# Performance work log

Hardware: AMD Instinct MI355X
Metric: run time of the kernel (lower is better)

The kernel has to match this reference:

```python
import jax, jax.numpy as jnp
import numpy as np

N_NODES = 50000
N_EDGES = 800000
IN_CH, HID_CH, OUT_CH, HEADS = 64, 32, 64, 8
NEG_SLOPE = 0.2


def setup_inputs() -> dict:
    key = jax.random.key(0)
    ks = jax.random.split(key, 12)
    x = jax.random.normal(ks[0], (N_NODES, IN_CH), dtype=jnp.float32)
    src = jax.random.randint(ks[1], (N_EDGES,), 0, N_NODES)
    dst = jax.random.randint(ks[2], (N_EDGES,), 0, N_NODES)
    edge_index = jnp.stack([src, dst]).astype(jnp.int64)
    g1 = 1.0 / np.sqrt(IN_CH)
    g2 = 1.0 / np.sqrt(HID_CH * HEADS)
    W1 = jax.random.normal(ks[3], (IN_CH, HEADS * HID_CH), dtype=jnp.float32) * g1
    a1_src = jax.random.normal(ks[4], (HEADS, HID_CH), dtype=jnp.float32) * g1
    a1_dst = jax.random.normal(ks[5], (HEADS, HID_CH), dtype=jnp.float32) * g1
    b1 = jnp.zeros((HEADS * HID_CH,), dtype=jnp.float32)
    W2 = jax.random.normal(ks[6], (HEADS * HID_CH, OUT_CH), dtype=jnp.float32) * g2
    a2_src = jax.random.normal(ks[7], (1, OUT_CH), dtype=jnp.float32) * g2
    a2_dst = jax.random.normal(ks[8], (1, OUT_CH), dtype=jnp.float32) * g2
    b2 = jnp.zeros((OUT_CH,), dtype=jnp.float32)
    return {"x": x, "edge_index": edge_index, "W1": W1, "a1_src": a1_src,
            "a1_dst": a1_dst, "b1": b1, "W2": W2, "a2_src": a2_src,
            "a2_dst": a2_dst, "b2": b2}


def _gat_conv(x, src, dst, W, a_s, a_d, b, heads, out_ch, concat):
    """PyG GATConv: per-head linear, edge attention, segment softmax, scatter-add."""
    n = x.shape[0]
    h = (x @ W).reshape(n, heads, out_ch)                    # [N,H,C]
    al_s = jnp.einsum('nhc,hc->nh', h, a_s)                  # [N,H]
    al_d = jnp.einsum('nhc,hc->nh', h, a_d)
    e = jax.nn.leaky_relu(al_s[src] + al_d[dst], NEG_SLOPE)  # [E,H]
    m = jax.ops.segment_max(e, dst, num_segments=n)          # [N,H]
    m = jnp.where(jnp.isfinite(m), m, 0.0)
    ex = jnp.exp(e - m[dst])
    denom = jax.ops.segment_sum(ex, dst, num_segments=n)
    alpha = ex / (denom[dst] + 1e-16)                        # [E,H]
    msg = h[src] * alpha[:, :, None]                         # [E,H,C]
    out = jax.ops.segment_sum(msg, dst, num_segments=n)      # [N,H,C]
    out = out.reshape(n, heads * out_ch) if concat else out.mean(axis=1)
    return out + b


def reference(x, edge_index, W1, a1_src, a1_dst, b1, W2, a2_src, a2_dst, b2):
    n = x.shape[0]
    loops = jnp.arange(n, dtype=edge_index.dtype)
    src = jnp.concatenate([edge_index[0], loops])  # self-loops (PyG default)
    dst = jnp.concatenate([edge_index[1], loops])
    h = _gat_conv(x, src, dst, W1, a1_src, a1_dst, b1, HEADS, HID_CH, True)
    h = jax.nn.elu(h)
    return _gat_conv(h, src, dst, W2, a2_src, a2_dst, b2, 1, OUT_CH, False)
```

## Files before the change

kernel.cpp:

```cpp
#include <hip/hip_runtime.h>
#include <hip/hip_fp16.h>

#define NEG_SLOPE 0.2f
#define EPB 4096
#define CAP_B 2560

__global__ __launch_bounds__(256, 4) void k_phase1(
    const int* __restrict__ ei, int E,
    const float* __restrict__ x, const float* __restrict__ W1,
    const float* __restrict__ a1s, const float* __restrict__ a1d,
    __half* __restrict__ h1h, float* __restrict__ al1s, float* __restrict__ al1d,
    int* __restrict__ cursor, unsigned* __restrict__ pairs,
    int n, int nbuck, int nP1B)
{
  __shared__ int sh[2048];
  int t = threadIdx.x;
  if (blockIdx.x < nP1B) {
    int* hist = sh;
    int* hbase = sh + 512;
    for (int i = t; i < nbuck; i += 256) hist[i] = 0;
    __syncthreads();
    int ebase = blockIdx.x * EPB;
    int pk[16], bk[16], rk[16];
#pragma unroll
    for (int k = 0; k < 16; k++) {
      int eid = ebase + k * 256 + t;
      bk[k] = -1; pk[k] = 0; rk[k] = 0;
      if (eid < E) {
        int s = ei[eid], d = ei[E + eid];
        s = (s < 0) ? 0 : (s >= n ? n - 1 : s);
        d = (d < 0) ? 0 : (d >= n ? n - 1 : d);
        bk[k] = d >> 7;
        pk[k] = ((d & 127) << 17) | s;
        rk[k] = atomicAdd(&hist[d >> 7], 1);
      }
    }
    __syncthreads();
    for (int b = t; b < nbuck; b += 256) {
      int c = hist[b];
      hbase[b] = c ? atomicAdd(&cursor[b], c) : 0;
    }
    __syncthreads();
#pragma unroll
    for (int k = 0; k < 16; k++) {
      if (bk[k] >= 0) {
        int idx = hbase[bk[k]] + rk[k];
        if (idx < CAP_B)
          pairs[(size_t)bk[k] * CAP_B + idx] = (unsigned)pk[k];
      }
    }
    return;
  }
  float (*xs)[64] = reinterpret_cast<float(*)[64]>(sh);
  int cg = t & 63;
  int mg = t >> 6;
  int base = (blockIdx.x - nP1B) * 32;
  for (int i = t; i < 32 * 16; i += 256) {
    int m = i >> 4, k4 = i & 15;
    int node = base + m;
    float4 v = make_float4(0.f, 0.f, 0.f, 0.f);
    if (node < n) v = reinterpret_cast<const float4*>(x + (size_t)node * 64)[k4];
    reinterpret_cast<float4*>(&xs[m][0])[k4] = v;
  }
  float4 as4 = reinterpret_cast<const float4*>(a1s)[cg];
  float4 ad4 = reinterpret_cast<const float4*>(a1d)[cg];
  __syncthreads();
  float4 acc[8];
#pragma unroll
  for (int m = 0; m < 8; m++) acc[m] = make_float4(0.f, 0.f, 0.f, 0.f);
#pragma unroll 1
  for (int k4 = 0; k4 < 16; k4++) {
    float4 w0 = reinterpret_cast<const float4*>(W1 + (size_t)(4 * k4 + 0) * 256)[cg];
    float4 w1 = reinterpret_cast<const float4*>(W1 + (size_t)(4 * k4 + 1) * 256)[cg];
    float4 w2 = reinterpret_cast<const float4*>(W1 + (size_t)(4 * k4 + 2) * 256)[cg];
    float4 w3 = reinterpret_cast<const float4*>(W1 + (size_t)(4 * k4 + 3) * 256)[cg];
#pragma unroll
    for (int m = 0; m < 8; m++) {
      float4 xv = reinterpret_cast<float4*>(&xs[mg * 8 + m][0])[k4];
      acc[m].x = fmaf(xv.x, w0.x, acc[m].x); acc[m].y = fmaf(xv.x, w0.y, acc[m].y);
      acc[m].z = fmaf(xv.x, w0.z, acc[m].z); acc[m].w = fmaf(xv.x, w0.w, acc[m].w);
      acc[m].x = fmaf(xv.y, w1.x, acc[m].x); acc[m].y = fmaf(xv.y, w1.y, acc[m].y);
      acc[m].z = fmaf(xv.y, w1.z, acc[m].z); acc[m].w = fmaf(xv.y, w1.w, acc[m].w);
      acc[m].x = fmaf(xv.z, w2.x, acc[m].x); acc[m].y = fmaf(xv.z, w2.y, acc[m].y);
      acc[m].z = fmaf(xv.z, w2.z, acc[m].z); acc[m].w = fmaf(xv.z, w2.w, acc[m].w);
      acc[m].x = fmaf(xv.w, w3.x, acc[m].x); acc[m].y = fmaf(xv.w, w3.y, acc[m].y);
      acc[m].z = fmaf(xv.w, w3.z, acc[m].z); acc[m].w = fmaf(xv.w, w3.w, acc[m].w);
    }
  }
#pragma unroll
  for (int m = 0; m < 8; m++) {
    int node = base + mg * 8 + m;
    if (node < n) {
      int head = cg >> 3;
      __half2 p01 = __floats2half2_rn(acc[m].x, acc[m].y);
      __half2 p23 = __floats2half2_rn(acc[m].z, acc[m].w);
      uint2 pko;
      pko.x = *reinterpret_cast<unsigned int*>(&p01);
      pko.y = *reinterpret_cast<unsigned int*>(&p23);
      reinterpret_cast<uint2*>(h1h + (size_t)head * n * 32 + (size_t)node * 32)[cg & 7] = pko;
      float s_ = acc[m].x * as4.x + acc[m].y * as4.y + acc[m].z * as4.z + acc[m].w * as4.w;
      float d_ = acc[m].x * ad4.x + acc[m].y * ad4.y + acc[m].z * ad4.z + acc[m].w * ad4.w;
      s_ += __shfl_xor(s_, 1); d_ += __shfl_xor(d_, 1);
      s_ += __shfl_xor(s_, 2); d_ += __shfl_xor(d_, 2);
      s_ += __shfl_xor(s_, 4); d_ += __shfl_xor(d_, 4);
      if ((cg & 7) == 0) {
        al1s[(size_t)head * n + node] = s_;
        al1d[(size_t)head * n + node] = d_;
      }
    }
  }
}

__global__ __launch_bounds__(256) void k_pass2(
    const unsigned* __restrict__ pairs, const int* __restrict__ cursor,
    int* __restrict__ gcur, int* __restrict__ deg, int* __restrict__ rowoff,
    int* __restrict__ csr, int n)
{
  __shared__ int cnt[128], off[128], rk[128];
  __shared__ int bbase;
  int b = blockIdx.x, t = threadIdx.x;
  if (t < 128) { cnt[t] = 0; rk[t] = 0; }
  __syncthreads();
  int total = min(cursor[b], CAP_B);
  size_t base = (size_t)b * CAP_B;
  for (int i = t; i < total; i += 256)
    atomicAdd(&cnt[pairs[base + i] >> 17], 1);
  __syncthreads();
  if (t == 0) {
    int run = 0;
    for (int i = 0; i < 128; i++) { off[i] = run; run += cnt[i]; }
    bbase = atomicAdd(gcur, run);
  }
  __syncthreads();
  int bb = bbase;
  if (t < 128) {
    int node = (b << 7) + t;
    if (node < n) { deg[node] = cnt[t]; rowoff[node] = bb + off[t]; }
  }
  for (int i = t; i < total; i += 256) {
    unsigned p = pairs[base + i];
    int local = p >> 17;
    int slot = atomicAdd(&rk[local], 1);
    csr[bb + off[local] + slot] = (int)(p & 0x1FFFF);
  }
}

__global__ __launch_bounds__(256, 4) void k_linear2(
    const __half* __restrict__ hacth, const float* __restrict__ W2,
    const float* __restrict__ a2s, const float* __restrict__ a2d,
    __half* __restrict__ h2h, float* __restrict__ al2s, float* __restrict__ al2d,
    int n)
{
  __shared__ float xs[32][260];
  int t = threadIdx.x;
  int cg = t & 15;
  int mg = t >> 4;
  int base = blockIdx.x * 32;
  for (int i = t; i < 32 * 32; i += 256) {
    int m = i >> 5, c8 = i & 31;
    int node = base + m;
    uint4 pk = make_uint4(0, 0, 0, 0);
    if (node < n) pk = reinterpret_cast<const uint4*>(hacth + (size_t)node * 256)[c8];
    __half2* hp = reinterpret_cast<__half2*>(&pk);
    float2 f0 = __half22float2(hp[0]);
    float2 f1 = __half22float2(hp[1]);
    float2 f2 = __half22float2(hp[2]);
    float2 f3 = __half22float2(hp[3]);
    float4* dst = reinterpret_cast<float4*>(&xs[m][c8 * 8]);
    dst[0] = make_float4(f0.x, f0.y, f1.x, f1.y);
    dst[1] = make_float4(f2.x, f2.y, f3.x, f3.y);
  }
  float4 as4 = reinterpret_cast<const float4*>(a2s)[cg];
  float4 ad4 = reinterpret_cast<const float4*>(a2d)[cg];
  __syncthreads();
  float4 a0 = make_float4(0.f, 0.f, 0.f, 0.f);
  float4 a1 = make_float4(0.f, 0.f, 0.f, 0.f);
#pragma unroll 2
  for (int k4 = 0; k4 < 64; k4++) {
    float4 w0 = reinterpret_cast<const float4*>(W2 + (size_t)(4 * k4 + 0) * 64)[cg];
    float4 w1 = reinterpret_cast<const float4*>(W2 + (size_t)(4 * k4 + 1) * 64)[cg];
    float4 w2 = reinterpret_cast<const float4*>(W2 + (size_t)(4 * k4 + 2) * 64)[cg];
    float4 w3 = reinterpret_cast<const float4*>(W2 + (size_t)(4 * k4 + 3) * 64)[cg];
    float4 x0 = *reinterpret_cast<float4*>(&xs[2 * mg + 0][k4 * 4]);
    float4 x1 = *reinterpret_cast<float4*>(&xs[2 * mg + 1][k4 * 4]);
    a0.x = fmaf(x0.x, w0.x, a0.x); a0.y = fmaf(x0.x, w0.y, a0.y);
    a0.z = fmaf(x0.x, w0.z, a0.z); a0.w = fmaf(x0.x, w0.w, a0.w);
    a0.x = fmaf(x0.y, w1.x, a0.x); a0.y = fmaf(x0.y, w1.y, a0.y);
    a0.z = fmaf(x0.y, w1.z, a0.z); a0.w = fmaf(x0.y, w1.w, a0.w);
    a0.x = fmaf(x0.z, w2.x, a0.x); a0.y = fmaf(x0.z, w2.y, a0.y);
    a0.z = fmaf(x0.z, w2.z, a0.z); a0.w = fmaf(x0.z, w2.w, a0.w);
    a0.x = fmaf(x0.w, w3.x, a0.x); a0.y = fmaf(x0.w, w3.y, a0.y);
    a0.z = fmaf(x0.w, w3.z, a0.z); a0.w = fmaf(x0.w, w3.w, a0.w);
    a1.x = fmaf(x1.x, w0.x, a1.x); a1.y = fmaf(x1.x, w0.y, a1.y);
    a1.z = fmaf(x1.x, w0.z, a1.z); a1.w = fmaf(x1.x, w0.w, a1.w);
    a1.x = fmaf(x1.y, w1.x, a1.x); a1.y = fmaf(x1.y, w1.y, a1.y);
    a1.z = fmaf(x1.y, w1.z, a1.z); a1.w = fmaf(x1.y, w1.w, a1.w);
    a1.x = fmaf(x1.z, w2.x, a1.x); a1.y = fmaf(x1.z, w2.y, a1.y);
    a1.z = fmaf(x1.z, w2.z, a1.z); a1.w = fmaf(x1.z, w2.w, a1.w);
    a1.x = fmaf(x1.w, w3.x, a1.x); a1.y = fmaf(x1.w, w3.y, a1.y);
    a1.z = fmaf(x1.w, w3.z, a1.z); a1.w = fmaf(x1.w, w3.w, a1.w);
  }
#pragma unroll
  for (int nd = 0; nd < 2; nd++) {
    float4 a = nd ? a1 : a0;
    int node = base + 2 * mg + nd;
    if (node < n) {
      __half2 q0 = __floats2half2_rn(a.x, a.y);
      __half2 q1 = __floats2half2_rn(a.z, a.w);
      uint2 pk;
      pk.x = *reinterpret_cast<unsigned int*>(&q0);
      pk.y = *reinterpret_cast<unsigned int*>(&q1);
      reinterpret_cast<uint2*>(h2h + (size_t)node * 64)[cg] = pk;
      float s_ = a.x * as4.x + a.y * as4.y + a.z * as4.z + a.w * as4.w;
      float d_ = a.x * ad4.x + a.y * ad4.y + a.z * ad4.z + a.w * ad4.w;
      s_ += __shfl_xor(s_, 1); d_ += __shfl_xor(d_, 1);
      s_ += __shfl_xor(s_, 2); d_ += __shfl_xor(d_, 2);
      s_ += __shfl_xor(s_, 4); d_ += __shfl_xor(d_, 4);
      s_ += __shfl_xor(s_, 8); d_ += __shfl_xor(d_, 8);
      if (cg == 0) { al2s[node] = s_; al2d[node] = d_; }
    }
  }
}

__global__ __launch_bounds__(256) void k_gather1(
    const __half* __restrict__ h1h, const float* __restrict__ al1s, const float* __restrict__ al1d,
    const int* __restrict__ degv, const int* __restrict__ rowoff, const int* __restrict__ csr,
    const float* __restrict__ b1, __half* __restrict__ hacth, int n)
{
  int head = blockIdx.x & 7;
  int node = ((blockIdx.x >> 3) << 6) + (threadIdx.x >> 2);
  if (node >= n) return;
  int q = threadIdx.x & 2 ? (threadIdx.x & 3) : (threadIdx.x & 3);
  q = threadIdx.x & 3;
  const __half* slab = h1h + (size_t)head * n * 32;
  const float* als = al1s + (size_t)head * n;
  float ald = al1d[(size_t)head * n + node];
  int beg = rowoff[node];
  int deg = degv[node];
  uint4 nr = reinterpret_cast<const uint4*>(slab + (size_t)node * 32)[q];
  float eS = als[node] + ald;
  eS = eS > 0.f ? eS : NEG_SLOPE * eS;
  float exS = __expf(eS);
  float acc[8];
#pragma unroll
  for (int k = 0; k < 8; k++) acc[k] = 0.f;
  float den = 0.f;
  if (deg > 0) {
    int sA = csr[beg];
    float alA = als[sA];
    uint4 pa = reinterpret_cast<const uint4*>(slab + (size_t)sA * 32)[q];
    for (int i = 0; i < deg; i++) {
      float alB = 0.f;
      uint4 pb = make_uint4(0, 0, 0, 0);
      if (i + 1 < deg) {
        int sB = csr[beg + i + 1];
        alB = als[sB];
        pb = reinterpret_cast<const uint4*>(slab + (size_t)sB * 32)[q];
      }
      float e = alA + ald;
      e = e > 0.f ? e : NEG_SLOPE * e;
      float ex = __expf(e);
      den += ex;
      __half2* hp = reinterpret_cast<__half2*>(&pa);
#pragma unroll
      for (int j = 0; j < 4; j++) {
        float2 f = __half22float2(hp[j]);
        acc[2 * j + 0] = fmaf(ex, f.x, acc[2 * j + 0]);
        acc[2 * j + 1] = fmaf(ex, f.y, acc[2 * j + 1]);
      }
      alA = alB; pa = pb;
    }
  }
  den += exS;
  {
    __half2* hp = reinterpret_cast<__half2*>(&nr);
#pragma unroll
    for (int j = 0; j < 4; j++) {
      float2 f = __half22float2(hp[j]);
      acc[2 * j + 0] = fmaf(exS, f.x, acc[2 * j + 0]);
      acc[2 * j + 1] = fmaf(exS, f.y, acc[2 * j + 1]);
    }
  }
  float inv = 1.f / (den + 1e-16f);
  float4 b40 = reinterpret_cast<const float4*>(b1 + head * 32)[2 * q];
  float4 b41 = reinterpret_cast<const float4*>(b1 + head * 32)[2 * q + 1];
  float o[8];
  o[0] = acc[0] * inv + b40.x; o[1] = acc[1] * inv + b40.y;
  o[2] = acc[2] * inv + b40.z; o[3] = acc[3] * inv + b40.w;
  o[4] = acc[4] * inv + b41.x; o[5] = acc[5] * inv + b41.y;
  o[6] = acc[6] * inv + b41.z; o[7] = acc[7] * inv + b41.w;
#pragma unroll
  for (int k = 0; k < 8; k++) o[k] = o[k] > 0.f ? o[k] : (__expf(o[k]) - 1.f);
  uint4 w0;
  __half2 t0, t1;
  t0 = __floats2half2_rn(o[0], o[1]);  w0.x = *reinterpret_cast<unsigned int*>(&t0);
  t1 = __floats2half2_rn(o[2], o[3]);  w0.y = *reinterpret_cast<unsigned int*>(&t1);
  t0 = __floats2half2_rn(o[4], o[5]);  w0.z = *reinterpret_cast<unsigned int*>(&t0);
  t1 = __floats2half2_rn(o[6], o[7]);  w0.w = *reinterpret_cast<unsigned int*>(&t1);
  *reinterpret_cast<uint4*>(hacth + (size_t)node * 256 + head * 32 + q * 8) = w0;
}

__global__ __launch_bounds__(256) void k_gather2(
    const __half* __restrict__ h2h, const float* __restrict__ al2s, const float* __restrict__ al2d,
    const int* __restrict__ degv, const int* __restrict__ rowoff, const int* __restrict__ csr,
    const float* __restrict__ b2, float* __restrict__ out, int n)
{
  int node = blockIdx.x * 32 + (threadIdx.x >> 3);
  if (node >= n) return;
  int q = threadIdx.x & 7;
  int beg = rowoff[node];
  int deg = degv[node];
  float ald = al2d[node];
  uint4 pN = reinterpret_cast<const uint4*>(h2h + (size_t)node * 64)[q];
  float eS = al2s[node] + ald;
  eS = eS > 0.f ? eS : NEG_SLOPE * eS;
  float exS = __expf(eS);
  float acc[8];
#pragma unroll
  for (int k = 0; k < 8; k++) acc[k] = 0.f;
  float den = 0.f;
  if (deg > 0) {
    int sA = csr[beg];
    float alA = al2s[sA];
    uint4 pA = reinterpret_cast<const uint4*>(h2h + (size_t)sA * 64)[q];
    for (int i = 0; i < deg; i++) {
      float alB = 0.f;
      uint4 pB = make_uint4(0, 0, 0, 0);
      if (i + 1 < deg) {
        int sB = csr[beg + i + 1];
        alB = al2s[sB];
        pB = reinterpret_cast<const uint4*>(h2h + (size_t)sB * 64)[q];
      }
      float e = alA + ald;
      e = e > 0.f ? e : NEG_SLOPE * e;
      float ex = __expf(e);
      den += ex;
      __half2* hp = reinterpret_cast<__half2*>(&pA);
#pragma unroll
      for (int j = 0; j < 4; j++) {
        float2 f = __half22float2(hp[j]);
        acc[2 * j + 0] = fmaf(ex, f.x, acc[2 * j + 0]);
        acc[2 * j + 1] = fmaf(ex, f.y, acc[2 * j + 1]);
      }
      alA = alB; pA = pB;
    }
  }
  den += exS;
  {
    __half2* hp = reinterpret_cast<__half2*>(&pN);
#pragma unroll
    for (int j = 0; j < 4; j++) {
      float2 f = __half22float2(hp[j]);
      acc[2 * j + 0] = fmaf(exS, f.x, acc[2 * j + 0]);
      acc[2 * j + 1] = fmaf(exS, f.y, acc[2 * j + 1]);
    }
  }
  float inv = 1.f / (den + 1e-16f);
  float4 b40 = reinterpret_cast<const float4*>(b2)[2 * q];
  float4 b41 = reinterpret_cast<const float4*>(b2)[2 * q + 1];
  float4 o0, o1;
  o0.x = acc[0] * inv + b40.x; o0.y = acc[1] * inv + b40.y;
  o0.z = acc[2] * inv + b40.z; o0.w = acc[3] * inv + b40.w;
  o1.x = acc[4] * inv + b41.x; o1.y = acc[5] * inv + b41.y;
  o1.z = acc[6] * inv + b41.z; o1.w = acc[7] * inv + b41.w;
  float4* orow = reinterpret_cast<float4*>(out + (size_t)node * 64);
  orow[2 * q] = o0; orow[2 * q + 1] = o1;
}

extern "C" void kernel_launch(void* const* d_in, const int* in_sizes, int n_in,
                              void* d_out, int out_size, void* d_ws, size_t ws_size,
                              hipStream_t stream)
{
  const float* x        = (const float*)d_in[0];
  const int*   ei       = (const int*)d_in[1];
  const float* W1       = (const float*)d_in[2];
  const float* a1s      = (const float*)d_in[3];
  const float* a1d      = (const float*)d_in[4];
  const float* b1       = (const float*)d_in[5];
  const float* W2       = (const float*)d_in[6];
  const float* a2s      = (const float*)d_in[7];
  const float* a2d      = (const float*)d_in[8];
  const float* b2       = (const float*)d_in[9];
  float* out            = (float*)d_out;

  int N  = in_sizes[0] / 64;
  int E  = in_sizes[1] / 2;
  int NBUCK = (N + 127) >> 7;

  char* p = (char*)d_ws;
  auto alloc = [&](size_t bytes) -> char* {
    char* r = p;
    p += (bytes + 255) & ~(size_t)255;
    return r;
  };
  __half* h1h    = (__half*)alloc((size_t)N * 256 * 2);
  __half* hacth  = (__half*)alloc((size_t)N * 256 * 2);
  float* al1s    = (float*)alloc((size_t)N * 8 * 4);
  float* al1d    = (float*)alloc((size_t)N * 8 * 4);
  float* al2s    = (float*)alloc((size_t)N * 4);
  float* al2d    = (float*)alloc((size_t)N * 4);
  int*   deg     = (int*)alloc((size_t)N * 4);
  int*   rowoff  = (int*)alloc((size_t)N * 4);
  int*   csr     = (int*)alloc((size_t)NBUCK * CAP_B * 4);
  unsigned* pairs = (unsigned*)alloc((size_t)NBUCK * CAP_B * 4);
  int*   cursor  = (int*)alloc((size_t)(NBUCK + 1) * 4);
  int*   gcur    = cursor + NBUCK;
  __half* h2h    = h1h;

  hipMemsetAsync(cursor, 0, (size_t)(NBUCK + 1) * 4, stream);

  int nP1B = (E + EPB - 1) / EPB;
  int nLB = (N + 31) / 32;
  k_phase1<<<nP1B + nLB, 256, 0, stream>>>(ei, E, x, W1, a1s, a1d,
                                           h1h, al1s, al1d, cursor, pairs, N, NBUCK, nP1B);
  k_pass2<<<NBUCK, 256, 0, stream>>>(pairs, cursor, gcur, deg, rowoff, csr, N);
  int nG1 = 8 * ((N + 63) / 64);
  k_gather1<<<nG1, 256, 0, stream>>>(h1h, al1s, al1d, deg, rowoff, csr, b1, hacth, N);
  k_linear2<<<(N + 31) / 32, 256, 0, stream>>>(hacth, W2, a2s, a2d, h2h, al2s, al2d, N);
  k_gather2<<<(N + 31) / 32, 256, 0, stream>>>(h2h, al2s, al2d, deg, rowoff, csr, b2, out, N);
}
```

Measured before the change: 232.7 us.

## Split layer-2 features into channel slabs and widen per-thread gather work

Layer-2 linear output is now stored as two 32-channel half-precision slabs, so gather2 splits channels across blocks the way gather1 splits heads, giving a smaller per-slab working set for the random row reads. Both gather kernels now use 2 threads per node with 16 channels each instead of 4 or 8 threads, and prefetch the next CSR index one step further ahead. The CSR index loads and the output stores become nontemporal. This cuts redundant index and attention-logit loads per lane, at the cost of more registers per thread and fewer threads per node.

After: 323.8 us. +39.2%, slower.

```diff
diff --git a/kernel.cpp b/kernel.cpp
--- a/kernel.cpp
+++ b/kernel.cpp
@@ -4,6 +4,9 @@
 #define NEG_SLOPE 0.2f
 #define EPB 4096
 #define CAP_B 2560
+
+typedef unsigned int uint4v __attribute__((ext_vector_type(4)));
+typedef float float4v __attribute__((ext_vector_type(4)));
 
 __global__ __launch_bounds__(256, 4) void k_phase1(
     const int* __restrict__ ei, int E,
@@ -210,7 +213,7 @@
       uint2 pk;
       pk.x = *reinterpret_cast<unsigned int*>(&q0);
       pk.y = *reinterpret_cast<unsigned int*>(&q1);
-      reinterpret_cast<uint2*>(h2h + (size_t)node * 64)[cg] = pk;
+      reinterpret_cast<uint2*>(h2h + (size_t)(cg >> 3) * n * 32 + (size_t)node * 32)[cg & 7] = pk;
       float s_ = a.x * as4.x + a.y * as4.y + a.z * as4.z + a.w * as4.w;
       float d_ = a.x * ad4.x + a.y * ad4.y + a.z * ad4.z + a.w * ad4.w;
       s_ += __shfl_xor(s_, 1); d_ += __shfl_xor(d_, 1);
@@ -228,76 +231,97 @@
     const float* __restrict__ b1, __half* __restrict__ hacth, int n)
 {
   int head = blockIdx.x & 7;
-  int node = ((blockIdx.x >> 3) << 6) + (threadIdx.x >> 2);
+  int node = ((blockIdx.x >> 3) << 7) + (threadIdx.x >> 1);
   if (node >= n) return;
-  int q = threadIdx.x & 2 ? (threadIdx.x & 3) : (threadIdx.x & 3);
-  q = threadIdx.x & 3;
+  int q = threadIdx.x & 1;
   const __half* slab = h1h + (size_t)head * n * 32;
   const float* als = al1s + (size_t)head * n;
   float ald = al1d[(size_t)head * n + node];
   int beg = rowoff[node];
   int deg = degv[node];
-  uint4 nr = reinterpret_cast<const uint4*>(slab + (size_t)node * 32)[q];
+  const uint4* rowN = reinterpret_cast<const uint4*>(slab + (size_t)node * 32);
+  uint4 n0 = rowN[2 * q], n1 = rowN[2 * q + 1];
   float eS = als[node] + ald;
   eS = eS > 0.f ? eS : NEG_SLOPE * eS;
   float exS = __expf(eS);
-  float acc[8];
-#pragma unroll
-  for (int k = 0; k < 8; k++) acc[k] = 0.f;
+  float acc[16];
+#pragma unroll
+  for (int k = 0; k < 16; k++) acc[k] = 0.f;
   float den = 0.f;
   if (deg > 0) {
-    int sA = csr[beg];
-    float alA = als[sA];
-    uint4 pa = reinterpret_cast<const uint4*>(slab + (size_t)sA * 32)[q];
+    int s1 = (deg > 1) ? __builtin_nontemporal_load(csr + beg + 1) : 0;
+    int s0 = __builtin_nontemporal_load(csr + beg);
+    float alA = als[s0];
+    const uint4* rA = reinterpret_cast<const uint4*>(slab + (size_t)s0 * 32);
+    uint4 pa0 = rA[2 * q], pa1 = rA[2 * q + 1];
     for (int i = 0; i < deg; i++) {
+      int sN = 0;
+      if (i + 2 < deg) sN = __builtin_nontemporal_load(csr + beg + i + 2);
       float alB = 0.f;
-      uint4 pb = make_uint4(0, 0, 0, 0);
+      uint4 pb0 = make_uint4(0, 0, 0, 0), pb1 = make_uint4(0, 0, 0, 0);
       if (i + 1 < deg) {
-        int sB = csr[beg + i + 1];
-        alB = als[sB];
-        pb = reinterpret_cast<const uint4*>(slab + (size_t)sB * 32)[q];
+        alB = als[s1];
+        const uint4* rB = reinterpret_cast<const uint4*>(slab + (size_t)s1 * 32);
+        pb0 = rB[2 * q]; pb1 = rB[2 * q + 1];
       }
       float e = alA + ald;
       e = e > 0.f ? e : NEG_SLOPE * e;
       float ex = __expf(e);
       den += ex;
-      __half2* hp = reinterpret_cast<__half2*>(&pa);
+      __half2* hp0 = reinterpret_cast<__half2*>(&pa0);
+      __half2* hp1 = reinterpret_cast<__half2*>(&pa1);
 #pragma unroll
       for (int j = 0; j < 4; j++) {
-        float2 f = __half22float2(hp[j]);
-        acc[2 * j + 0] = fmaf(ex, f.x, acc[2 * j + 0]);
-        acc[2 * j + 1] = fmaf(ex, f.y, acc[2 * j + 1]);
-      }
-      alA = alB; pa = pb;
+        float2 f0 = __half22float2(hp0[j]);
+        float2 f1 = __half22float2(hp1[j]);
+        acc[2 * j + 0] = fmaf(ex, f0.x, acc[2 * j + 0]);
+        acc[2 * j + 1] = fmaf(ex, f0.y, acc[2 * j + 1]);
+        acc[8 + 2 * j + 0] = fmaf(ex, f1.x, acc[8 + 2 * j + 0]);
+        acc[8 + 2 * j + 1] = fmaf(ex, f1.y, acc[8 + 2 * j + 1]);
+      }
+      alA = alB; pa0 = pb0; pa1 = pb1; s1 = sN;
     }
   }
   den += exS;
   {
-    __half2* hp = reinterpret_cast<__half2*>(&nr);
+    __half2* hp0 = reinterpret_cast<__half2*>(&n0);
+    __half2* hp1 = reinterpret_cast<__half2*>(&n1);
 #pragma unroll
     for (int j = 0; j < 4; j++) {
-      float2 f = __half22float2(hp[j]);
-      acc[2 * j + 0] = fmaf(exS, f.x, acc[2 * j + 0]);
-      acc[2 * j + 1] = fmaf(exS, f.y, acc[2 * j + 1]);
+      float2 f0 = __half22float2(hp0[j]);
+      float2 f1 = __half22float2(hp1[j]);
+      acc[2 * j + 0] = fmaf(exS, f0.x, acc[2 * j + 0]);
+      acc[2 * j + 1] = fmaf(exS, f0.y, acc[2 * j + 1]);
+      acc[8 + 2 * j + 0] = fmaf(exS, f1.x, acc[8 + 2 * j + 0]);
+      acc[8 + 2 * j + 1] = fmaf(exS, f1.y, acc[8 + 2 * j + 1]);
     }
   }
   float inv = 1.f / (den + 1e-16f);
-  float4 b40 = reinterpret_cast<const float4*>(b1 + head * 32)[2 * q];
-  float4 b41 = reinterpret_cast<const float4*>(b1 + head * 32)[2 * q + 1];
-  float o[8];
-  o[0] = acc[0] * inv + b40.x; o[1] = acc[1] * inv + b40.y;
-  o[2] = acc[2] * inv + b40.z; o[3] = acc[3] * inv + b40.w;
-  o[4] = acc[4] * inv + b41.x; o[5] = acc[5] * inv + b41.y;
-  o[6] = acc[6] * inv + b41.z; o[7] = acc[7] * inv + b41.w;
-#pragma unroll
-  for (int k = 0; k < 8; k++) o[k] = o[k] > 0.f ? o[k] : (__expf(o[k]) - 1.f);
-  uint4 w0;
+  const float4* bb = reinterpret_cast<const float4*>(b1 + head * 32);
+  float o[16];
+#pragma unroll
+  for (int j = 0; j < 4; j++) {
+    float4 b4 = bb[4 * q + j];
+    o[4 * j + 0] = acc[4 * j + 0] * inv + b4.x;
+    o[4 * j + 1] = acc[4 * j + 1] * inv + b4.y;
+    o[4 * j + 2] = acc[4 * j + 2] * inv + b4.z;
+    o[4 * j + 3] = acc[4 * j + 3] * inv + b4.w;
+  }
+#pragma unroll
+  for (int k = 0; k < 16; k++) o[k] = o[k] > 0.f ? o[k] : (__expf(o[k]) - 1.f);
+  uint4v w0, w1;
   __half2 t0, t1;
-  t0 = __floats2half2_rn(o[0], o[1]);  w0.x = *reinterpret_cast<unsigned int*>(&t0);
-  t1 = __floats2half2_rn(o[2], o[3]);  w0.y = *reinterpret_cast<unsigned int*>(&t1);
-  t0 = __floats2half2_rn(o[4], o[5]);  w0.z = *reinterpret_cast<unsigned int*>(&t0);
-  t1 = __floats2half2_rn(o[6], o[7]);  w0.w = *reinterpret_cast<unsigned int*>(&t1);
-  *reinterpret_cast<uint4*>(hacth + (size_t)node * 256 + head * 32 + q * 8) = w0;
+  t0 = __floats2half2_rn(o[0], o[1]);   w0.x = *reinterpret_cast<unsigned int*>(&t0);
+  t1 = __floats2half2_rn(o[2], o[3]);   w0.y = *reinterpret_cast<unsigned int*>(&t1);
+  t0 = __floats2half2_rn(o[4], o[5]);   w0.z = *reinterpret_cast<unsigned int*>(&t0);
+  t1 = __floats2half2_rn(o[6], o[7]);   w0.w = *reinterpret_cast<unsigned int*>(&t1);
+  t0 = __floats2half2_rn(o[8], o[9]);   w1.x = *reinterpret_cast<unsigned int*>(&t0);
+  t1 = __floats2half2_rn(o[10], o[11]); w1.y = *reinterpret_cast<unsigned int*>(&t1);
+  t0 = __floats2half2_rn(o[12], o[13]); w1.z = *reinterpret_cast<unsigned int*>(&t0);
+  t1 = __floats2half2_rn(o[14], o[15]); w1.w = *reinterpret_cast<unsigned int*>(&t1);
+  uint4v* orow = reinterpret_cast<uint4v*>(hacth + (size_t)node * 256 + head * 32 + q * 16);
+  __builtin_nontemporal_store(w0, orow);
+  __builtin_nontemporal_store(w1, orow + 1);
 }
 
 __global__ __launch_bounds__(256) void k_gather2(
@@ -305,66 +329,84 @@
     const int* __restrict__ degv, const int* __restrict__ rowoff, const int* __restrict__ csr,
     const float* __restrict__ b2, float* __restrict__ out, int n)
 {
-  int node = blockIdx.x * 32 + (threadIdx.x >> 3);
+  int c = blockIdx.x & 1;
+  int node = ((blockIdx.x >> 1) << 7) + (threadIdx.x >> 1);
   if (node >= n) return;
-  int q = threadIdx.x & 7;
+  int q = threadIdx.x & 1;
+  const __half* slab = h2h + (size_t)c * n * 32;
+  float ald = al2d[node];
   int beg = rowoff[node];
   int deg = degv[node];
-  float ald = al2d[node];
-  uint4 pN = reinterpret_cast<const uint4*>(h2h + (size_t)node * 64)[q];
+  const uint4* rowN = reinterpret_cast<const uint4*>(slab + (size_t)node * 32);
+  uint4 n0 = rowN[2 * q], n1 = rowN[2 * q + 1];
   float eS = al2s[node] + ald;
   eS = eS > 0.f ? eS : NEG_SLOPE * eS;
   float exS = __expf(eS);
-  float acc[8];
-#pragma unroll
-  for (int k = 0; k < 8; k++) acc[k] = 0.f;
+  float acc[16];
+#pragma unroll
+  for (int k = 0; k < 16; k++) acc[k] = 0.f;
   float den = 0.f;
   if (deg > 0) {
-    int sA = csr[beg];
-    float alA = al2s[sA];
-    uint4 pA = reinterpret_cast<const uint4*>(h2h + (size_t)sA * 64)[q];
+    int s1 = (deg > 1) ? __builtin_nontemporal_load(csr + beg + 1) : 0;
+    int s0 = __builtin_nontemporal_load(csr + beg);
+    float alA = al2s[s0];
+    const uint4* rA = reinterpret_cast<const uint4*>(slab + (size_t)s0 * 32);
+    uint4 pa0 = rA[2 * q], pa1 = rA[2 * q + 1];
     for (int i = 0; i < deg; i++) {
+      int sN = 0;
+      if (i + 2 < deg) sN = __builtin_nontemporal_load(csr + beg + i + 2);
       float alB = 0.f;
-      uint4 pB = make_uint4(0, 0, 0, 0);
+      uint4 pb0 = make_uint4(0, 0, 0, 0), pb1 = make_uint4(0, 0, 0, 0);
       if (i + 1 < deg) {
-        int sB = csr[beg + i + 1];
-        alB = al2s[sB];
-        pB = reinterpret_cast<const uint4*>(h2h + (size_t)sB * 64)[q];
+        alB = al2s[s1];
+        const uint4* rB = reinterpret_cast<const uint4*>(slab + (size_t)s1 * 32);
+        pb0 = rB[2 * q]; pb1 = rB[2 * q + 1];
       }
       float e = alA + ald;
       e = e > 0.f ? e : NEG_SLOPE * e;
       float ex = __expf(e);
       den += ex;
-      __half2* hp = reinterpret_cast<__half2*>(&pA);
+      __half2* hp0 = reinterpret_cast<__half2*>(&pa0);
+      __half2* hp1 = reinterpret_cast<__half2*>(&pa1);
 #pragma unroll
       for (int j = 0; j < 4; j++) {
-        float2 f = __half22float2(hp[j]);
-        acc[2 * j + 0] = fmaf(ex, f.x, acc[2 * j + 0]);
-        acc[2 * j + 1] = fmaf(ex, f.y, acc[2 * j + 1]);
-      }
-      alA = alB; pA = pB;
+        float2 f0 = __half22float2(hp0[j]);
+        float2 f1 = __half22float2(hp1[j]);
+        acc[2 * j + 0] = fmaf(ex, f0.x, acc[2 * j + 0]);
+        acc[2 * j + 1] = fmaf(ex, f0.y, acc[2 * j + 1]);
+        acc[8 + 2 * j + 0] = fmaf(ex, f1.x, acc[8 + 2 * j + 0]);
+        acc[8 + 2 * j + 1] = fmaf(ex, f1.y, acc[8 + 2 * j + 1]);
+      }
+      alA = alB; pa0 = pb0; pa1 = pb1; s1 = sN;
     }
   }
   den += exS;
   {
-    __half2* hp = reinterpret_cast<__half2*>(&pN);
+    __half2* hp0 = reinterpret_cast<__half2*>(&n0);
+    __half2* hp1 = reinterpret_cast<__half2*>(&n1);
 #pragma unroll
     for (int j = 0; j < 4; j++) {
-      float2 f = __half22float2(hp[j]);
-      acc[2 * j + 0] = fmaf(exS, f.x, acc[2 * j + 0]);
-      acc[2 * j + 1] = fmaf(exS, f.y, acc[2 * j + 1]);
+      float2 f0 = __half22float2(hp0[j]);
+      float2 f1 = __half22float2(hp1[j]);
+      acc[2 * j + 0] = fmaf(exS, f0.x, acc[2 * j + 0]);
+      acc[2 * j + 1] = fmaf(exS, f0.y, acc[2 * j + 1]);
+      acc[8 + 2 * j + 0] = fmaf(exS, f1.x, acc[8 + 2 * j + 0]);
+      acc[8 + 2 * j + 1] = fmaf(exS, f1.y, acc[8 + 2 * j + 1]);
     }
   }
   float inv = 1.f / (den + 1e-16f);
-  float4 b40 = reinterpret_cast<const float4*>(b2)[2 * q];
-  float4 b41 = reinterpret_cast<const float4*>(b2)[2 * q + 1];
-  float4 o0, o1;
-  o0.x = acc[0] * inv + b40.x; o0.y = acc[1] * inv + b40.y;
-  o0.z = acc[2] * inv + b40.z; o0.w = acc[3] * inv + b40.w;
-  o1.x = acc[4] * inv + b41.x; o1.y = acc[5] * inv + b41.y;
-  o1.z = acc[6] * inv + b41.z; o1.w = acc[7] * inv + b41.w;
-  float4* orow = reinterpret_cast<float4*>(out + (size_t)node * 64);
-  orow[2 * q] = o0; orow[2 * q + 1] = o1;
+  const float4* bb = reinterpret_cast<const float4*>(b2 + c * 32);
+  float* op = out + (size_t)node * 64 + c * 32 + q * 16;
+#pragma unroll
+  for (int j = 0; j < 4; j++) {
+    float4 b4 = bb[4 * q + j];
+    float4v o4;
+    o4.x = acc[4 * j + 0] * inv + b4.x;
+    o4.y = acc[4 * j + 1] * inv + b4.y;
+    o4.z = acc[4 * j + 2] * inv + b4.z;
+    o4.w = acc[4 * j + 3] * inv + b4.w;
+    __builtin_nontemporal_store(o4, reinterpret_cast<float4v*>(op) + j);
+  }
 }
 
 extern "C" void kernel_launch(void* const* d_in, const int* in_sizes, int n_in,
@@ -414,8 +456,9 @@
   k_phase1<<<nP1B + nLB, 256, 0, stream>>>(ei, E, x, W1, a1s, a1d,
                                            h1h, al1s, al1d, cursor, pairs, N, NBUCK, nP1B);
   k_pass2<<<NBUCK, 256, 0, stream>>>(pairs, cursor, gcur, deg, rowoff, csr, N);
-  int nG1 = 8 * ((N + 63) / 64);
+  int nG1 = 8 * ((N + 127) / 128);
   k_gather1<<<nG1, 256, 0, stream>>>(h1h, al1s, al1d, deg, rowoff, csr, b1, hacth, N);
   k_linear2<<<(N + 31) / 32, 256, 0, stream>>>(hacth, W2, a2s, a2d, h2h, al2s, al2d, N);
-  k_gather2<<<(N + 31) / 32, 256, 0, stream>>>(h2h, al2s, al2d, deg, rowoff, csr, b2, out, N);
-}
+  int nG2 = 2 * ((N + 127) / 128);
+  k_gather2<<<nG2, 256, 0, stream>>>(h2h, al2s, al2d, deg, rowoff, csr, b2, out, N);
+}
```

## Split layer-2 features into column slabs and deepen gather prefetch

Applied to the files above, without the earlier changes.

Layer-2 features are now stored as two 32-column half-precision slabs instead of one 64-wide row. Gather2 is split so each block processes one slab for 64 nodes, mirroring the per-head slab layout of gather1, which shrinks the random-access footprint per block and may improve L2 locality. Both gathers now prefetch two neighbours ahead and load the CSR index three ahead, to hide more load latency at the cost of extra registers. Outputs are written with nontemporal stores. Gather2 now reads neighbour indices and attention scores twice, once per slab.

Result: faster. 221.7 us (-4.7%).

```diff
diff --git a/kernel.cpp b/kernel.cpp
--- a/kernel.cpp
+++ b/kernel.cpp
@@ -4,6 +4,9 @@
 #define NEG_SLOPE 0.2f
 #define EPB 4096
 #define CAP_B 2560
+
+typedef unsigned int uint4v __attribute__((ext_vector_type(4)));
+typedef float float4v __attribute__((ext_vector_type(4)));
 
 __global__ __launch_bounds__(256, 4) void k_phase1(
     const int* __restrict__ ei, int E,
@@ -210,7 +213,7 @@
       uint2 pk;
       pk.x = *reinterpret_cast<unsigned int*>(&q0);
       pk.y = *reinterpret_cast<unsigned int*>(&q1);
-      reinterpret_cast<uint2*>(h2h + (size_t)node * 64)[cg] = pk;
+      reinterpret_cast<uint2*>(h2h + (size_t)(cg >> 3) * n * 32 + (size_t)node * 32)[cg & 7] = pk;
       float s_ = a.x * as4.x + a.y * as4.y + a.z * as4.z + a.w * as4.w;
       float d_ = a.x * ad4.x + a.y * ad4.y + a.z * ad4.z + a.w * ad4.w;
       s_ += __shfl_xor(s_, 1); d_ += __shfl_xor(d_, 1);
@@ -230,8 +233,7 @@
   int head = blockIdx.x & 7;
   int node = ((blockIdx.x >> 3) << 6) + (threadIdx.x >> 2);
   if (node >= n) return;
-  int q = threadIdx.x & 2 ? (threadIdx.x & 3) : (threadIdx.x & 3);
-  q = threadIdx.x & 3;
+  int q = threadIdx.x & 3;
   const __half* slab = h1h + (size_t)head * n * 32;
   const float* als = al1s + (size_t)head * n;
   float ald = al1d[(size_t)head * n + node];
@@ -246,29 +248,37 @@
   for (int k = 0; k < 8; k++) acc[k] = 0.f;
   float den = 0.f;
   if (deg > 0) {
-    int sA = csr[beg];
-    float alA = als[sA];
-    uint4 pa = reinterpret_cast<const uint4*>(slab + (size_t)sA * 32)[q];
+    int s0 = csr[beg];
+    int s1 = (deg > 1) ? csr[beg + 1] : 0;
+    int s2 = (deg > 2) ? csr[beg + 2] : 0;
+    float alA = als[s0];
+    uint4 pA = reinterpret_cast<const uint4*>(slab + (size_t)s0 * 32)[q];
+    float alB = 0.f;
+    uint4 pB = make_uint4(0, 0, 0, 0);
+    if (deg > 1) {
+      alB = als[s1];
+      pB = reinterpret_cast<const uint4*>(slab + (size_t)s1 * 32)[q];
+    }
     for (int i = 0; i < deg; i++) {
-      float alB = 0.f;
-      uint4 pb = make_uint4(0, 0, 0, 0);
-      if (i + 1 < deg) {
-        int sB = csr[beg + i + 1];
-        alB = als[sB];
-        pb = reinterpret_cast<const uint4*>(slab + (size_t)sB * 32)[q];
-      }
+      float alC = 0.f;
+      uint4 pC = make_uint4(0, 0, 0, 0);
+      if (i + 2 < deg) {
+        alC = als[s2];
+        pC = reinterpret_cast<const uint4*>(slab + (size_t)s2 * 32)[q];
+      }
+      int s3 = (i + 3 < deg) ? csr[beg + i + 3] : 0;
       float e = alA + ald;
       e = e > 0.f ? e : NEG_SLOPE * e;
       float ex = __expf(e);
       den += ex;
-      __half2* hp = reinterpret_cast<__half2*>(&pa);
+      __half2* hp = reinterpret_cast<__half2*>(&pA);
 #pragma unroll
       for (int j = 0; j < 4; j++) {
         float2 f = __half22float2(hp[j]);
         acc[2 * j + 0] = fmaf(ex, f.x, acc[2 * j + 0]);
         acc[2 * j + 1] = fmaf(ex, f.y, acc[2 * j + 1]);
       }
-      alA = alB; pa = pb;
+      alA = alB; pA = pB; alB = alC; pB = pC; s2 = s3;
     }
   }
   den += exS;
@@ -282,8 +292,8 @@
     }
   }
   float inv = 1.f / (den + 1e-16f);
-  float4 b40 = reinterpret_cast<const float4*>(b1 + head * 32)[2 * q];
-  float4 b41 = reinterpret_cast<const float4*>(b1 + head * 32)[2 * q + 1];
+  const float4* bb = reinterpret_cast<const float4*>(b1 + head * 32);
+  float4 b40 = bb[2 * q], b41 = bb[2 * q + 1];
   float o[8];
   o[0] = acc[0] * inv + b40.x; o[1] = acc[1] * inv + b40.y;
   o[2] = acc[2] * inv + b40.z; o[3] = acc[3] * inv + b40.w;
@@ -291,13 +301,14 @@
   o[6] = acc[6] * inv + b41.z; o[7] = acc[7] * inv + b41.w;
 #pragma unroll
   for (int k = 0; k < 8; k++) o[k] = o[k] > 0.f ? o[k] : (__expf(o[k]) - 1.f);
-  uint4 w0;
+  uint4v w0;
   __half2 t0, t1;
   t0 = __floats2half2_rn(o[0], o[1]);  w0.x = *reinterpret_cast<unsigned int*>(&t0);
   t1 = __floats2half2_rn(o[2], o[3]);  w0.y = *reinterpret_cast<unsigned int*>(&t1);
   t0 = __floats2half2_rn(o[4], o[5]);  w0.z = *reinterpret_cast<unsigned int*>(&t0);
   t1 = __floats2half2_rn(o[6], o[7]);  w0.w = *reinterpret_cast<unsigned int*>(&t1);
-  *reinterpret_cast<uint4*>(hacth + (size_t)node * 256 + head * 32 + q * 8) = w0;
+  __builtin_nontemporal_store(
+      w0, reinterpret_cast<uint4v*>(hacth + (size_t)node * 256 + head * 32 + q * 8));
 }
 
 __global__ __launch_bounds__(256) void k_gather2(
@@ -305,13 +316,15 @@
     const int* __restrict__ degv, const int* __restrict__ rowoff, const int* __restrict__ csr,
     const float* __restrict__ b2, float* __restrict__ out, int n)
 {
-  int node = blockIdx.x * 32 + (threadIdx.x >> 3);
+  int c = blockIdx.x & 1;
+  int node = ((blockIdx.x >> 1) << 6) + (threadIdx.x >> 2);
   if (node >= n) return;
-  int q = threadIdx.x & 7;
+  int q = threadIdx.x & 3;
+  const __half* slab = h2h + (size_t)c * n * 32;
+  float ald = al2d[node];
   int beg = rowoff[node];
   int deg = degv[node];
-  float ald = al2d[node];
-  uint4 pN = reinterpret_cast<const uint4*>(h2h + (size_t)node * 64)[q];
+  uint4 nr = reinterpret_cast<const uint4*>(slab + (size_t)node * 32)[q];
   float eS = al2s[node] + ald;
   eS = eS > 0.f ? eS : NEG_SLOPE * eS;
   float exS = __expf(eS);
@@ -320,17 +333,25 @@
   for (int k = 0; k < 8; k++) acc[k] = 0.f;
   float den = 0.f;
   if (deg > 0) {
-    int sA = csr[beg];
-    float alA = al2s[sA];
-    uint4 pA = reinterpret_cast<const uint4*>(h2h + (size_t)sA * 64)[q];
+    int s0 = csr[beg];
+    int s1 = (deg > 1) ? csr[beg + 1] : 0;
+    int s2 = (deg > 2) ? csr[beg + 2] : 0;
+    float alA = al2s[s0];
+    uint4 pA = reinterpret_cast<const uint4*>(slab + (size_t)s0 * 32)[q];
+    float alB = 0.f;
+    uint4 pB = make_uint4(0, 0, 0, 0);
+    if (deg > 1) {
+      alB = al2s[s1];
+      pB = reinterpret_cast<const uint4*>(slab + (size_t)s1 * 32)[q];
+    }
     for (int i = 0; i < deg; i++) {
-      float alB = 0.f;
-      uint4 pB = make_uint4(0, 0, 0, 0);
-      if (i + 1 < deg) {
-        int sB = csr[beg + i + 1];
-        alB = al2s[sB];
-        pB = reinterpret_cast<const uint4*>(h2h + (size_t)sB * 64)[q];
-      }
+      float alC = 0.f;
+      uint4 pC = make_uint4(0, 0, 0, 0);
+      if (i + 2 < deg) {
+        alC = al2s[s2];
+        pC = reinterpret_cast<const uint4*>(slab + (size_t)s2 * 32)[q];
+      }
+      int s3 = (i + 3 < deg) ? csr[beg + i + 3] : 0;
       float e = alA + ald;
       e = e > 0.f ? e : NEG_SLOPE * e;
       float ex = __expf(e);
@@ -342,12 +363,12 @@
         acc[2 * j + 0] = fmaf(ex, f.x, acc[2 * j + 0]);
         acc[2 * j + 1] = fmaf(ex, f.y, acc[2 * j + 1]);
       }
-      alA = alB; pA = pB;
+      alA = alB; pA = pB; alB = alC; pB = pC; s2 = s3;
     }
   }
   den += exS;
   {
-    __half2* hp = reinterpret_cast<__half2*>(&pN);
+    __half2* hp = reinterpret_cast<__half2*>(&nr);
 #pragma unroll
     for (int j = 0; j < 4; j++) {
       float2 f = __half22float2(hp[j]);
@@ -356,15 +377,16 @@
     }
   }
   float inv = 1.f / (den + 1e-16f);
-  float4 b40 = reinterpret_cast<const float4*>(b2)[2 * q];
-  float4 b41 = reinterpret_cast<const float4*>(b2)[2 * q + 1];
-  float4 o0, o1;
+  const float4* bb = reinterpret_cast<const float4*>(b2 + c * 32);
+  float4 b40 = bb[2 * q], b41 = bb[2 * q + 1];
+  float* op = out + (size_t)node * 64 + c * 32 + q * 8;
+  float4v o0, o1;
   o0.x = acc[0] * inv + b40.x; o0.y = acc[1] * inv + b40.y;
   o0.z = acc[2] * inv + b40.z; o0.w = acc[3] * inv + b40.w;
   o1.x = acc[4] * inv + b41.x; o1.y = acc[5] * inv + b41.y;
   o1.z = acc[6] * inv + b41.z; o1.w = acc[7] * inv + b41.w;
-  float4* orow = reinterpret_cast<float4*>(out + (size_t)node * 64);
-  orow[2 * q] = o0; orow[2 * q + 1] = o1;
+  __builtin_nontemporal_store(o0, reinterpret_cast<float4v*>(op));
+  __builtin_nontemporal_store(o1, reinterpret_cast<float4v*>(op) + 1);
 }
 
 extern "C" void kernel_launch(void* const* d_in, const int* in_sizes, int n_in,
@@ -417,5 +439,6 @@
   int nG1 = 8 * ((N + 63) / 64);
   k_gather1<<<nG1, 256, 0, stream>>>(h1h, al1s, al1d, deg, rowoff, csr, b1, hacth, N);
   k_linear2<<<(N + 31) / 32, 256, 0, stream>>>(hacth, W2, a2s, a2d, h2h, al2s, al2d, N);
-  k_gather2<<<(N + 31) / 32, 256, 0, stream>>>(h2h, al2s, al2d, deg, rowoff, csr, b2, out, N);
-}
+  int nG2 = 2 * ((N + 63) / 64);
+  k_gather2<<<nG2, 256, 0, stream>>>(h2h, al2s, al2d, deg, rowoff, csr, b2, out, N);
+}
```
